# Performance work log

Hardware: AMD Instinct MI355X
Metric: run time of the kernel (lower is better)

## Reference

```python
import jax, jax.numpy as jnp
import numpy as np

N, E, C = 50000, 600000, 128
BN_EPS = 1e-5
NORM_EPS = 1e-12


def _edgeconv(x, src, dst, wa, ba, g, be, rm, rv, wb, bb):
    # PyG EdgeConv: message = MLP(concat(x_i, x_j - x_i)); aggr='add' at target i
    x_i = x[dst]                      # [E, C] target features
    x_j = x[src]                      # [E, C] source features
    m = jnp.concatenate([x_i, x_j - x_i], axis=-1)   # [E, 2C]
    m = jax.nn.relu(m @ wa.T + ba)                   # Linear(2C->C) + ReLU
    m = (m - rm) * (g * jax.lax.rsqrt(rv + BN_EPS)) + be  # BatchNorm1d (eval)
    m = m @ wb.T + bb                                # Linear(C->C)
    return jax.ops.segment_sum(m, dst, num_segments=x.shape[0])  # [N, C]


def _lin(k, fan_in, shape):
    bound = 1.0 / np.sqrt(fan_in)
    return jax.random.uniform(k, shape, jnp.float32, -bound, bound)


def setup_inputs() -> dict:
    key = jax.random.key(0)
    ks = jax.random.split(key, 16)
    inp = {
        "x": jax.random.normal(ks[0], (N, C), jnp.float32),
        "edge_index": jax.random.randint(ks[1], (2, E), 0, N, jnp.int64),
    }
    # layer 1 params
    inp["w1a"] = _lin(ks[2], 2 * C, (C, 2 * C)); inp["b1a"] = _lin(ks[3], 2 * C, (C,))
    inp["g1"] = jnp.ones((C,), jnp.float32) + 0.1 * jax.random.normal(ks[4], (C,))
    inp["be1"] = 0.1 * jax.random.normal(ks[5], (C,))
    inp["rm1"] = 0.1 * jax.random.normal(ks[6], (C,))
    inp["rv1"] = 0.5 + jax.random.uniform(ks[7], (C,))
    inp["w1b"] = _lin(ks[8], C, (C, C)); inp["b1b"] = _lin(ks[9], C, (C,))
    # layer 2 params
    inp["w2a"] = _lin(ks[10], 2 * C, (C, 2 * C)); inp["b2a"] = _lin(ks[11], 2 * C, (C,))
    inp["g2"] = jnp.ones((C,), jnp.float32) + 0.1 * jax.random.normal(ks[12], (C,))
    inp["be2"] = 0.1 * jax.random.normal(ks[13], (C,))
    inp["rm2"] = 0.1 * jax.random.normal(ks[14], (C,))
    inp["rv2"] = 0.5 + jax.random.uniform(ks[15], (C,))
    k2 = jax.random.split(ks[15], 2)
    inp["w2b"] = _lin(k2[0], C, (C, C)); inp["b2b"] = _lin(k2[1], C, (C,))
    return inp


def reference(x, edge_index, w1a, b1a, g1, be1, rm1, rv1, w1b, b1b,
              w2a, b2a, g2, be2, rm2, rv2, w2b, b2b):
    src, dst = edge_index[0], edge_index[1]
    # layer 1 (all but last): conv -> relu -> L2 normalize -> dropout(eval=identity)
    h = _edgeconv(x, src, dst, w1a, b1a, g1, be1, rm1, rv1, w1b, b1b)
    h = jax.nn.relu(h)
    h = h / jnp.maximum(jnp.linalg.norm(h, axis=-1, keepdims=True), NORM_EPS)
    # last layer: conv only
    return _edgeconv(h, src, dst, w2a, b2a, g2, be2, rm2, rv2, w2b, b2b)
```

## Files before the change

kernel.cpp:

```cpp
#include <hip/hip_runtime.h>

#define CCH 128
#define WPAD 136
typedef unsigned short ushort;
typedef __attribute__((ext_vector_type(8))) short bf16x8_t;
typedef __attribute__((ext_vector_type(4))) float f32x4;

union ABu { bf16x8_t v; ushort u[8]; uint4 q; };

__device__ __forceinline__ ushort f2b(float f) {
  union { float f; unsigned u; } v{f};
  unsigned r = v.u + 0x7fffu + ((v.u >> 16) & 1u);
  return (ushort)(r >> 16);
}
__device__ __forceinline__ float b2f(ushort s) {
  union { unsigned u; float f; } v{(unsigned)s << 16};
  return v.f;
}

__global__ __launch_bounds__(256) void k_pre(const float* __restrict__ x,
                                             ushort* __restrict__ XB, int nxc,
                                             const float* __restrict__ w1a,
                                             const float* __restrict__ w1b,
                                             const float* __restrict__ w2a,
                                             const float* __restrict__ w2b,
                                             ushort* __restrict__ Wcat1, ushort* __restrict__ Wb1,
                                             ushort* __restrict__ Wcat2, ushort* __restrict__ Wb2,
                                             const void* __restrict__ ei, int* __restrict__ deg,
                                             int E, int xcb) {
  const int b = blockIdx.x, t = threadIdx.x;
  if (b < 128) {
    int i = b * 256 + t;
    int c = i >> 7, k = i & 127;
    float v = (c < 128) ? w1a[c * 256 + k] - w1a[c * 256 + 128 + k]
                        : w1a[(c - 128) * 256 + 128 + k];
    Wcat1[i] = f2b(v);
    if (i < 16384) Wb1[i] = f2b(w1b[i]);
  } else if (b < 256) {
    int i = (b - 128) * 256 + t;
    int c = i >> 7, k = i & 127;
    float v = (c < 128) ? w2a[c * 256 + k] - w2a[c * 256 + 128 + k]
                        : w2a[(c - 128) * 256 + 128 + k];
    Wcat2[i] = f2b(v);
    if (i < 16384) Wb2[i] = f2b(w2b[i]);
  } else if (b < 256 + xcb) {
    size_t i = (size_t)(b - 256) * 256 + t;
    if (i < (size_t)nxc) {
      const float* xp = x + i * 8;
      float4 f0 = *(const float4*)xp;
      float4 f1 = *(const float4*)(xp + 4);
      ushort o[8] = {f2b(f0.x), f2b(f0.y), f2b(f0.z), f2b(f0.w),
                     f2b(f1.x), f2b(f1.y), f2b(f1.z), f2b(f1.w)};
      *(uint4*)&XB[i * 8] = *(const uint4*)o;
    }
  } else {
    __shared__ int nz;
    if (t == 0) nz = 0;
    __syncthreads();
    int e = (b - 256 - xcb) * 256 + t;
    unsigned hi = (e < E) ? ((const unsigned*)ei)[2 * (size_t)e + 1] : 0u;
    if (hi) atomicAdd(&nz, 1);
    __syncthreads();
    bool i64 = (nz == 0);
    if (e < E) {
      int d = i64 ? (int)((const long long*)ei)[(size_t)E + e]
                  : ((const int*)ei)[(size_t)E + e];
      atomicAdd(&deg[d], 1);
    }
  }
}

__global__ __launch_bounds__(256) void k_rowptr(const int* __restrict__ deg,
                                                const int* __restrict__ bsum,
                                                int* __restrict__ rowptr,
                                                int n, int nb, int Etot) {
  __shared__ int s[256];
  const int t = threadIdx.x, b = blockIdx.x;
  s[t] = (t < nb && t < b) ? bsum[t] : 0;
  __syncthreads();
  for (int off = 128; off > 0; off >>= 1) {
    if (t < off) s[t] += s[t + off];
    __syncthreads();
  }
  int boffset = s[0];
  __syncthreads();
  int i = b * 256 + t;
  int v = (i < n) ? deg[i] : 0;
  s[t] = v; __syncthreads();
  for (int off = 1; off < 256; off <<= 1) {
    int tv = (t >= off) ? s[t - off] : 0;
    __syncthreads();
    s[t] += tv;
    __syncthreads();
  }
  if (i < n) rowptr[i] = boffset + s[t] - v;
  if (b == gridDim.x - 1 && t == 0) rowptr[n] = Etot;
}

__global__ __launch_bounds__(256) void k_scatter(const void* __restrict__ ei,
                                                 const int* __restrict__ rowptr,
                                                 int* __restrict__ cnt,
                                                 int* __restrict__ esrc, int E) {
  __shared__ int nz;
  const int t = threadIdx.x;
  if (t == 0) nz = 0;
  __syncthreads();
  int e = blockIdx.x * 256 + t;
  unsigned hi = (e < E) ? ((const unsigned*)ei)[2 * (size_t)e + 1] : 0u;
  if (hi) atomicAdd(&nz, 1);
  __syncthreads();
  bool i64 = (nz == 0);
  if (e < E) {
    int d, sv;
    if (i64) {
      sv = (int)((const long long*)ei)[(size_t)e];
      d  = (int)((const long long*)ei)[(size_t)E + e];
    } else {
      sv = ((const int*)ei)[(size_t)e];
      d  = ((const int*)ei)[(size_t)E + e];
    }
    int pos = rowptr[d] + atomicAdd(&cnt[d], 1);
    esrc[pos] = sv;
  }
}

__device__ __forceinline__ void gemm_core(const ushort* __restrict__ XB,
                                          const ushort* __restrict__ wlds,
                                          int rowb, int ln, int quad, int nN,
                                          f32x4 acc0[8], f32x4 acc1[8]) {
  const int ar0 = rowb + ln, ar1 = rowb + 16 + ln;
  ABu a0[4], a1[4];
#pragma unroll
  for (int kk = 0; kk < 4; ++kk) {
    a0[kk].q = (ar0 < nN) ? *(const uint4*)(XB + (size_t)ar0 * CCH + kk * 32 + quad * 8)
                          : make_uint4(0, 0, 0, 0);
    a1[kk].q = (ar1 < nN) ? *(const uint4*)(XB + (size_t)ar1 * CCH + kk * 32 + quad * 8)
                          : make_uint4(0, 0, 0, 0);
  }
#pragma unroll
  for (int s = 0; s < 8; ++s) {
    acc0[s] = (f32x4){0.f, 0.f, 0.f, 0.f};
    acc1[s] = (f32x4){0.f, 0.f, 0.f, 0.f};
  }
#pragma unroll
  for (int s = 0; s < 8; ++s) {
#pragma unroll
    for (int kk = 0; kk < 4; ++kk) {
      ABu b;
      b.q = *(const uint4*)&wlds[(s * 16 + ln) * WPAD + kk * 32 + quad * 8];
      acc0[s] = __builtin_amdgcn_mfma_f32_16x16x32_bf16(a0[kk].v, b.v, acc0[s], 0, 0, 0);
      acc1[s] = __builtin_amdgcn_mfma_f32_16x16x32_bf16(a1[kk].v, b.v, acc1[s], 0, 0, 0);
    }
  }
}

__device__ __forceinline__ void stage_w(const ushort* __restrict__ Wp,
                                        ushort* __restrict__ wlds, int t) {
  for (int i = t; i < 128 * 16; i += 256) {
    int row = i >> 4, ch = i & 15;
    *(uint4*)&wlds[row * WPAD + ch * 8] = *(const uint4*)&Wp[row * CCH + ch * 8];
  }
}

__device__ __forceinline__ void epi0(f32x4 acc[8], int rowb, int ln, int quad, int nN,
                                     const float* bias, int half, ushort* dst) {
#pragma unroll
  for (int s = 0; s < 8; ++s) {
    int col = s * 16 + ln;
    float bv = half ? 0.f : bias[col];
#pragma unroll
    for (int r = 0; r < 4; ++r) {
      int row = rowb + quad * 4 + r;
      if (row < nN) dst[(size_t)row * CCH + col] = f2b(acc[s][r] + bv);
    }
  }
}

__global__ __launch_bounds__(256) void k_mix1(const ushort* __restrict__ XB,
                                              const ushort* __restrict__ Wcat,
                                              const float* __restrict__ bias,
                                              ushort* __restrict__ A1,
                                              ushort* __restrict__ A2, int nN,
                                              const int* __restrict__ deg,
                                              int* __restrict__ bsum, int gH, int n) {
  __shared__ ushort wlds[128 * WPAD];
  const int t = threadIdx.x;
  if ((int)blockIdx.x >= 2 * gH) {
    int* s = (int*)wlds;
    int bb = blockIdx.x - 2 * gH;
    int i = bb * 256 + t;
    s[t] = (i < n) ? deg[i] : 0;
    __syncthreads();
    for (int off = 128; off > 0; off >>= 1) {
      if (t < off) s[t] += s[t + off];
      __syncthreads();
    }
    if (t == 0) bsum[bb] = s[0];
    return;
  }
  const int half = (int)blockIdx.x >= gH;
  const int bx = half ? blockIdx.x - gH : blockIdx.x;
  stage_w(Wcat + (size_t)half * 128 * CCH, wlds, t);
  __syncthreads();
  const int wave = t >> 6, lane = t & 63;
  const int ln = lane & 15, quad = lane >> 4;
  const int rowb = bx * 128 + wave * 32;
  f32x4 acc0[8], acc1[8];
  gemm_core(XB, wlds, rowb, ln, quad, nN, acc0, acc1);
  ushort* dst = half ? A2 : A1;
  epi0(acc0, rowb, ln, quad, nN, bias, half, dst);
  epi0(acc1, rowb + 16, ln, quad, nN, bias, half, dst);
}

template <int EPI>
__global__ __launch_bounds__(256) void k_gemm(const ushort* __restrict__ XB,
                                              const ushort* __restrict__ W,
                                              const float* __restrict__ bias,
                                              const int* __restrict__ deg,
                                              void* __restrict__ Y1,
                                              ushort* __restrict__ Y2, int nN) {
  __shared__ ushort wlds[128 * WPAD];
  const int t = threadIdx.x;
  const int half = (EPI == 0) ? blockIdx.y : 0;
  stage_w(W + (size_t)half * 128 * CCH, wlds, t);
  __syncthreads();
  const int wave = t >> 6, lane = t & 63;
  const int ln = lane & 15, quad = lane >> 4;
  const int rowb = blockIdx.x * 128 + wave * 32;
  f32x4 acc0[8], acc1[8];
  gemm_core(XB, wlds, rowb, ln, quad, nN, acc0, acc1);

  if constexpr (EPI == 0) {
    ushort* dst = half ? Y2 : (ushort*)Y1;
    epi0(acc0, rowb, ln, quad, nN, bias, half, dst);
    epi0(acc1, rowb + 16, ln, quad, nN, bias, half, dst);
  } else if constexpr (EPI == 1) {
    ushort* H = (ushort*)Y1;
    float biasv[8];
#pragma unroll
    for (int s = 0; s < 8; ++s) biasv[s] = bias[s * 16 + ln];
    auto epi = [&](f32x4* acc, int rb) {
#pragma unroll
      for (int r = 0; r < 4; ++r) {
        int row = rb + quad * 4 + r;
        float dn = (row < nN) ? (float)deg[row] : 0.f;
        float vals[8];
        float ss = 0.f;
#pragma unroll
        for (int s = 0; s < 8; ++s) {
          float v = fmaxf(acc[s][r] + dn * biasv[s], 0.f);
          vals[s] = v;
          ss += v * v;
        }
        ss += __shfl_xor(ss, 1, 64);
        ss += __shfl_xor(ss, 2, 64);
        ss += __shfl_xor(ss, 4, 64);
        ss += __shfl_xor(ss, 8, 64);
        float inv = 1.0f / fmaxf(sqrtf(ss), 1e-12f);
        if (row < nN) {
#pragma unroll
          for (int s = 0; s < 8; ++s)
            H[(size_t)row * CCH + s * 16 + ln] = f2b(vals[s] * inv);
        }
      }
    };
    epi(acc0, rowb); epi(acc1, rowb + 16);
  } else {
    float* OUT = (float*)Y1;
    float biasv[8];
#pragma unroll
    for (int s = 0; s < 8; ++s) biasv[s] = bias[s * 16 + ln];
    auto epi = [&](f32x4* acc, int rb) {
#pragma unroll
      for (int r = 0; r < 4; ++r) {
        int row = rb + quad * 4 + r;
        if (row >= nN) continue;
        float dn = (float)deg[row];
#pragma unroll
        for (int s = 0; s < 8; ++s)
          OUT[(size_t)row * CCH + s * 16 + ln] = acc[s][r] + dn * biasv[s];
      }
    };
    epi(acc0, rowb); epi(acc1, rowb + 16);
  }
}

__global__ __launch_bounds__(256) void k_aggr(const ushort* __restrict__ A1,
                                              const ushort* __restrict__ A2,
                                              const int* __restrict__ rowptr,
                                              const int* __restrict__ esrc,
                                              const float* __restrict__ g,
                                              const float* __restrict__ be,
                                              const float* __restrict__ rm,
                                              const float* __restrict__ rv,
                                              ushort* __restrict__ M, int nNodes) {
  int node = blockIdx.x * 4 + (threadIdx.x >> 6);
  if (node >= nNodes) return;
  int lane = threadIdx.x & 63;
  int q = lane >> 4;
  int c = (lane & 15) * 8;

  uint4 aq = *(const uint4*)&A1[(size_t)node * CCH + c];
  float a[8] = {b2f((ushort)aq.x), b2f((ushort)(aq.x >> 16)),
                b2f((ushort)aq.y), b2f((ushort)(aq.y >> 16)),
                b2f((ushort)aq.z), b2f((ushort)(aq.z >> 16)),
                b2f((ushort)aq.w), b2f((ushort)(aq.w >> 16))};
  int r0 = rowptr[node], r1 = rowptr[node + 1];
  float s[8] = {0.f, 0.f, 0.f, 0.f, 0.f, 0.f, 0.f, 0.f};

  auto acc8 = [&](uint4 w) {
    const unsigned* p = (const unsigned*)&w;
#pragma unroll
    for (int j = 0; j < 4; ++j) {
      s[2*j]   += fmaxf(a[2*j]   + b2f((ushort)p[j]), 0.f);
      s[2*j+1] += fmaxf(a[2*j+1] + b2f((ushort)(p[j] >> 16)), 0.f);
    }
  };

  for (int base = r0; base < r1; base += 64) {
    int navail = r1 - base; if (navail > 64) navail = 64;
    int myi = (lane < navail) ? esrc[base + lane] : 0;
    int g4 = navail >> 2, tail = navail & 3;
    int j = 0;
    for (; j + 4 <= g4; j += 4) {
      int p0 = j * 4 + q;
      int i0 = __shfl(myi, p0, 64);
      int i1 = __shfl(myi, p0 + 4, 64);
      int i2 = __shfl(myi, p0 + 8, 64);
      int i3 = __shfl(myi, p0 + 12, 64);
      uint4 w0 = *(const uint4*)&A2[(size_t)i0 * CCH + c];
      uint4 w1 = *(const uint4*)&A2[(size_t)i1 * CCH + c];
      uint4 w2 = *(const uint4*)&A2[(size_t)i2 * CCH + c];
      uint4 w3 = *(const uint4*)&A2[(size_t)i3 * CCH + c];
      acc8(w0); acc8(w1); acc8(w2); acc8(w3);
    }
    for (; j < g4; ++j) {
      int i0 = __shfl(myi, j * 4 + q, 64);
      acc8(*(const uint4*)&A2[(size_t)i0 * CCH + c]);
    }
    int pt = g4 * 4 + q; if (pt > 63) pt = 63;
    int it = __shfl(myi, pt, 64);
    if (q < tail) acc8(*(const uint4*)&A2[(size_t)it * CCH + c]);
  }
#pragma unroll
  for (int j = 0; j < 8; ++j) {
    s[j] += __shfl_xor(s[j], 16, 64);
    s[j] += __shfl_xor(s[j], 32, 64);
  }

  if (q == 0) {
    float dn = (float)(r1 - r0);
    unsigned p[4];
#pragma unroll
    for (int j = 0; j < 4; ++j) {
      float sc0 = g[c + 2*j]     * rsqrtf(rv[c + 2*j]     + 1e-5f);
      float sc1 = g[c + 2*j + 1] * rsqrtf(rv[c + 2*j + 1] + 1e-5f);
      float o0 = sc0 * s[2*j]     + dn * (be[c + 2*j]     - rm[c + 2*j]     * sc0);
      float o1 = sc1 * s[2*j + 1] + dn * (be[c + 2*j + 1] - rm[c + 2*j + 1] * sc1);
      p[j] = (unsigned)f2b(o0) | ((unsigned)f2b(o1) << 16);
    }
    *(uint4*)&M[(size_t)node * CCH + c] = make_uint4(p[0], p[1], p[2], p[3]);
  }
}

extern "C" void kernel_launch(void* const* d_in, const int* in_sizes, int n_in,
                              void* d_out, int out_size, void* d_ws, size_t ws_size,
                              hipStream_t stream) {
  const float* x   = (const float*)d_in[0];
  const void*  ei  = d_in[1];
  const float* w1a = (const float*)d_in[2];
  const float* b1a = (const float*)d_in[3];
  const float* g1  = (const float*)d_in[4];
  const float* be1 = (const float*)d_in[5];
  const float* rm1 = (const float*)d_in[6];
  const float* rv1 = (const float*)d_in[7];
  const float* w1b = (const float*)d_in[8];
  const float* b1b = (const float*)d_in[9];
  const float* w2a = (const float*)d_in[10];
  const float* b2a = (const float*)d_in[11];
  const float* g2  = (const float*)d_in[12];
  const float* be2 = (const float*)d_in[13];
  const float* rm2 = (const float*)d_in[14];
  const float* rv2 = (const float*)d_in[15];
  const float* w2b = (const float*)d_in[16];
  const float* b2b = (const float*)d_in[17];

  const int N = in_sizes[0] / CCH;
  const int E = in_sizes[1] / 2;
  const size_t NC = (size_t)N * CCH;

  int* deg    = (int*)d_ws;
  int* cnt    = deg + N;
  int* rowptr = cnt + N;
  int* bsum   = rowptr + N + 1;
  int* esrc   = bsum + 256;
  uintptr_t pw = ((uintptr_t)(esrc + E) + 63) & ~(uintptr_t)63;
  ushort* Wcat1 = (ushort*)pw;
  ushort* Wcat2 = Wcat1 + 32768;
  ushort* Wb1   = Wcat2 + 32768;
  ushort* Wb2   = Wb1 + 16384;
  uintptr_t pb = ((uintptr_t)(Wb2 + 16384) + 63) & ~(uintptr_t)63;
  ushort* XB = (ushort*)pb;
  ushort* B0 = XB + NC;
  ushort* B1 = B0 + NC;
  ushort* MB = B1 + NC;
  ushort* HB = MB + NC;

  const int gE  = (E + 255) / 256;
  const int gS  = (N + 255) / 256;
  const int gH  = (N + 127) / 128;
  const int gA  = (N + 3) / 4;
  const int nxc = (int)(NC / 8);
  const int xcb = (nxc + 255) / 256;

  hipMemsetAsync(deg, 0, sizeof(int) * 2 * (size_t)N, stream);
  k_pre<<<256 + xcb + gE, 256, 0, stream>>>(x, XB, nxc, w1a, w1b, w2a, w2b,
                                            Wcat1, Wb1, Wcat2, Wb2, ei, deg, E, xcb);
  k_mix1<<<2 * gH + gS, 256, 0, stream>>>(XB, Wcat1, b1a, B0, B1, N, deg, bsum, gH, N);
  k_rowptr<<<gS, 256, 0, stream>>>(deg, bsum, rowptr, N, gS, E);
  k_scatter<<<gE, 256, 0, stream>>>(ei, rowptr, cnt, esrc, E);

  k_aggr<<<gA, 256, 0, stream>>>(B0, B1, rowptr, esrc, g1, be1, rm1, rv1, MB, N);
  k_gemm<1><<<gH, 256, 0, stream>>>(MB, Wb1, b1b, deg, HB, nullptr, N);
  k_gemm<0><<<dim3(gH, 2), 256, 0, stream>>>(HB, Wcat2, b2a, deg, B0, B1, N);
  k_aggr<<<gA, 256, 0, stream>>>(B0, B1, rowptr, esrc, g2, be2, rm2, rv2, MB, N);
  k_gemm<2><<<gH, 256, 0, stream>>>(MB, Wb2, b2b, deg, d_out, nullptr, N);
}
```

Measured before the change: 299.3 us.

## Fuse fp32 input conversion into first GEMM and fuse layer-1 output GEMM with layer-2 input GEMM

Drops the separate x-to-bf16 conversion pass: k_mix1 now reads fp32 x and converts it in registers, and one block computes both weight halves so the A fragments are loaded once. Layer 1's Linear(C->C) with ReLU and L2-normalise now shares a kernel with layer 2's first GEMM. The normalised H stays in LDS rather than making a round trip through global memory, which also removes one launch. In exchange each block does more serial work, reuses the weight LDS buffer across stages with extra barriers, and k_fuse12 needs twice the LDS, which may lower occupancy.

Result: no change. 296.6 us (-0.9%).

```diff
diff --git a/kernel.cpp b/kernel.cpp
--- a/kernel.cpp
+++ b/kernel.cpp
@@ -18,16 +18,14 @@
   return v.f;
 }
 
-__global__ __launch_bounds__(256) void k_pre(const float* __restrict__ x,
-                                             ushort* __restrict__ XB, int nxc,
-                                             const float* __restrict__ w1a,
+__global__ __launch_bounds__(256) void k_pre(const float* __restrict__ w1a,
                                              const float* __restrict__ w1b,
                                              const float* __restrict__ w2a,
                                              const float* __restrict__ w2b,
                                              ushort* __restrict__ Wcat1, ushort* __restrict__ Wb1,
                                              ushort* __restrict__ Wcat2, ushort* __restrict__ Wb2,
                                              const void* __restrict__ ei, int* __restrict__ deg,
-                                             int E, int xcb) {
+                                             int E) {
   const int b = blockIdx.x, t = threadIdx.x;
   if (b < 128) {
     int i = b * 256 + t;
@@ -43,21 +41,11 @@
                         : w2a[(c - 128) * 256 + 128 + k];
     Wcat2[i] = f2b(v);
     if (i < 16384) Wb2[i] = f2b(w2b[i]);
-  } else if (b < 256 + xcb) {
-    size_t i = (size_t)(b - 256) * 256 + t;
-    if (i < (size_t)nxc) {
-      const float* xp = x + i * 8;
-      float4 f0 = *(const float4*)xp;
-      float4 f1 = *(const float4*)(xp + 4);
-      ushort o[8] = {f2b(f0.x), f2b(f0.y), f2b(f0.z), f2b(f0.w),
-                     f2b(f1.x), f2b(f1.y), f2b(f1.z), f2b(f1.w)};
-      *(uint4*)&XB[i * 8] = *(const uint4*)o;
-    }
   } else {
     __shared__ int nz;
     if (t == 0) nz = 0;
     __syncthreads();
-    int e = (b - 256 - xcb) * 256 + t;
+    int e = (b - 256) * 256 + t;
     unsigned hi = (e < E) ? ((const unsigned*)ei)[2 * (size_t)e + 1] : 0u;
     if (hi) atomicAdd(&nz, 1);
     __syncthreads();
@@ -124,12 +112,17 @@
   }
 }
 
-__device__ __forceinline__ void gemm_core(const ushort* __restrict__ XB,
-                                          const ushort* __restrict__ wlds,
-                                          int rowb, int ln, int quad, int nN,
-                                          f32x4 acc0[8], f32x4 acc1[8]) {
-  const int ar0 = rowb + ln, ar1 = rowb + 16 + ln;
-  ABu a0[4], a1[4];
+__device__ __forceinline__ void stage_w(const ushort* __restrict__ Wp,
+                                        ushort* __restrict__ wlds, int t) {
+  for (int i = t; i < 128 * 16; i += 256) {
+    int row = i >> 4, ch = i & 15;
+    *(uint4*)&wlds[row * WPAD + ch * 8] = *(const uint4*)&Wp[row * CCH + ch * 8];
+  }
+}
+
+__device__ __forceinline__ void load_a_bf16(const ushort* __restrict__ XB,
+                                            int ar0, int ar1, int quad, int nN,
+                                            ABu a0[4], ABu a1[4]) {
 #pragma unroll
   for (int kk = 0; kk < 4; ++kk) {
     a0[kk].q = (ar0 < nN) ? *(const uint4*)(XB + (size_t)ar0 * CCH + kk * 32 + quad * 8)
@@ -137,6 +130,46 @@
     a1[kk].q = (ar1 < nN) ? *(const uint4*)(XB + (size_t)ar1 * CCH + kk * 32 + quad * 8)
                           : make_uint4(0, 0, 0, 0);
   }
+}
+
+__device__ __forceinline__ void load_a_f32(const float* __restrict__ X,
+                                           int ar0, int ar1, int quad, int nN,
+                                           ABu a0[4], ABu a1[4]) {
+#pragma unroll
+  for (int kk = 0; kk < 4; ++kk) {
+    if (ar0 < nN) {
+      const float* p = X + (size_t)ar0 * CCH + kk * 32 + quad * 8;
+      float4 f0 = *(const float4*)p, f1 = *(const float4*)(p + 4);
+      a0[kk].u[0] = f2b(f0.x); a0[kk].u[1] = f2b(f0.y);
+      a0[kk].u[2] = f2b(f0.z); a0[kk].u[3] = f2b(f0.w);
+      a0[kk].u[4] = f2b(f1.x); a0[kk].u[5] = f2b(f1.y);
+      a0[kk].u[6] = f2b(f1.z); a0[kk].u[7] = f2b(f1.w);
+    } else a0[kk].q = make_uint4(0, 0, 0, 0);
+    if (ar1 < nN) {
+      const float* p = X + (size_t)ar1 * CCH + kk * 32 + quad * 8;
+      float4 f0 = *(const float4*)p, f1 = *(const float4*)(p + 4);
+      a1[kk].u[0] = f2b(f0.x); a1[kk].u[1] = f2b(f0.y);
+      a1[kk].u[2] = f2b(f0.z); a1[kk].u[3] = f2b(f0.w);
+      a1[kk].u[4] = f2b(f1.x); a1[kk].u[5] = f2b(f1.y);
+      a1[kk].u[6] = f2b(f1.z); a1[kk].u[7] = f2b(f1.w);
+    } else a1[kk].q = make_uint4(0, 0, 0, 0);
+  }
+}
+
+__device__ __forceinline__ void load_a_lds(const ushort* __restrict__ hlds,
+                                           int lr0, int lr1, int quad,
+                                           ABu a0[4], ABu a1[4]) {
+#pragma unroll
+  for (int kk = 0; kk < 4; ++kk) {
+    a0[kk].q = *(const uint4*)&hlds[lr0 * WPAD + kk * 32 + quad * 8];
+    a1[kk].q = *(const uint4*)&hlds[lr1 * WPAD + kk * 32 + quad * 8];
+  }
+}
+
+__device__ __forceinline__ void mma_tiles(const ABu a0[4], const ABu a1[4],
+                                          const ushort* __restrict__ wlds,
+                                          int ln, int quad,
+                                          f32x4 acc0[8], f32x4 acc1[8]) {
 #pragma unroll
   for (int s = 0; s < 8; ++s) {
     acc0[s] = (f32x4){0.f, 0.f, 0.f, 0.f};
@@ -154,14 +187,6 @@
   }
 }
 
-__device__ __forceinline__ void stage_w(const ushort* __restrict__ Wp,
-                                        ushort* __restrict__ wlds, int t) {
-  for (int i = t; i < 128 * 16; i += 256) {
-    int row = i >> 4, ch = i & 15;
-    *(uint4*)&wlds[row * WPAD + ch * 8] = *(const uint4*)&Wp[row * CCH + ch * 8];
-  }
-}
-
 __device__ __forceinline__ void epi0(f32x4 acc[8], int rowb, int ln, int quad, int nN,
                                      const float* bias, int half, ushort* dst) {
 #pragma unroll
@@ -176,7 +201,7 @@
   }
 }
 
-__global__ __launch_bounds__(256) void k_mix1(const ushort* __restrict__ XB,
+__global__ __launch_bounds__(256) void k_mix1(const float* __restrict__ x,
                                               const ushort* __restrict__ Wcat,
                                               const float* __restrict__ bias,
                                               ushort* __restrict__ A1,
@@ -185,9 +210,9 @@
                                               int* __restrict__ bsum, int gH, int n) {
   __shared__ ushort wlds[128 * WPAD];
   const int t = threadIdx.x;
-  if ((int)blockIdx.x >= 2 * gH) {
+  if ((int)blockIdx.x >= gH) {
     int* s = (int*)wlds;
-    int bb = blockIdx.x - 2 * gH;
+    int bb = blockIdx.x - gH;
     int i = bb * 256 + t;
     s[t] = (i < n) ? deg[i] : 0;
     __syncthreads();
@@ -198,91 +223,125 @@
     if (t == 0) bsum[bb] = s[0];
     return;
   }
-  const int half = (int)blockIdx.x >= gH;
-  const int bx = half ? blockIdx.x - gH : blockIdx.x;
-  stage_w(Wcat + (size_t)half * 128 * CCH, wlds, t);
-  __syncthreads();
-  const int wave = t >> 6, lane = t & 63;
-  const int ln = lane & 15, quad = lane >> 4;
-  const int rowb = bx * 128 + wave * 32;
-  f32x4 acc0[8], acc1[8];
-  gemm_core(XB, wlds, rowb, ln, quad, nN, acc0, acc1);
-  ushort* dst = half ? A2 : A1;
-  epi0(acc0, rowb, ln, quad, nN, bias, half, dst);
-  epi0(acc1, rowb + 16, ln, quad, nN, bias, half, dst);
-}
-
-template <int EPI>
-__global__ __launch_bounds__(256) void k_gemm(const ushort* __restrict__ XB,
-                                              const ushort* __restrict__ W,
-                                              const float* __restrict__ bias,
-                                              const int* __restrict__ deg,
-                                              void* __restrict__ Y1,
-                                              ushort* __restrict__ Y2, int nN) {
-  __shared__ ushort wlds[128 * WPAD];
-  const int t = threadIdx.x;
-  const int half = (EPI == 0) ? blockIdx.y : 0;
-  stage_w(W + (size_t)half * 128 * CCH, wlds, t);
-  __syncthreads();
   const int wave = t >> 6, lane = t & 63;
   const int ln = lane & 15, quad = lane >> 4;
   const int rowb = blockIdx.x * 128 + wave * 32;
+  stage_w(Wcat, wlds, t);
+  ABu a0[4], a1[4];
+  load_a_f32(x, rowb + ln, rowb + 16 + ln, quad, nN, a0, a1);
+  __syncthreads();
   f32x4 acc0[8], acc1[8];
-  gemm_core(XB, wlds, rowb, ln, quad, nN, acc0, acc1);
-
-  if constexpr (EPI == 0) {
-    ushort* dst = half ? Y2 : (ushort*)Y1;
-    epi0(acc0, rowb, ln, quad, nN, bias, half, dst);
-    epi0(acc1, rowb + 16, ln, quad, nN, bias, half, dst);
-  } else if constexpr (EPI == 1) {
-    ushort* H = (ushort*)Y1;
-    float biasv[8];
-#pragma unroll
-    for (int s = 0; s < 8; ++s) biasv[s] = bias[s * 16 + ln];
-    auto epi = [&](f32x4* acc, int rb) {
-#pragma unroll
-      for (int r = 0; r < 4; ++r) {
-        int row = rb + quad * 4 + r;
-        float dn = (row < nN) ? (float)deg[row] : 0.f;
-        float vals[8];
-        float ss = 0.f;
-#pragma unroll
-        for (int s = 0; s < 8; ++s) {
-          float v = fmaxf(acc[s][r] + dn * biasv[s], 0.f);
-          vals[s] = v;
-          ss += v * v;
-        }
-        ss += __shfl_xor(ss, 1, 64);
-        ss += __shfl_xor(ss, 2, 64);
-        ss += __shfl_xor(ss, 4, 64);
-        ss += __shfl_xor(ss, 8, 64);
-        float inv = 1.0f / fmaxf(sqrtf(ss), 1e-12f);
-        if (row < nN) {
-#pragma unroll
-          for (int s = 0; s < 8; ++s)
-            H[(size_t)row * CCH + s * 16 + ln] = f2b(vals[s] * inv);
-        }
+  mma_tiles(a0, a1, wlds, ln, quad, acc0, acc1);
+  epi0(acc0, rowb, ln, quad, nN, bias, 0, A1);
+  epi0(acc1, rowb + 16, ln, quad, nN, bias, 0, A1);
+  __syncthreads();
+  stage_w(Wcat + 128 * CCH, wlds, t);
+  __syncthreads();
+  mma_tiles(a0, a1, wlds, ln, quad, acc0, acc1);
+  epi0(acc0, rowb, ln, quad, nN, bias, 1, A2);
+  epi0(acc1, rowb + 16, ln, quad, nN, bias, 1, A2);
+}
+
+__global__ __launch_bounds__(256) void k_fuse12(const ushort* __restrict__ MB,
+                                                const ushort* __restrict__ Wb1,
+                                                const float* __restrict__ b1b,
+                                                const ushort* __restrict__ Wcat2,
+                                                const float* __restrict__ b2a,
+                                                const int* __restrict__ deg,
+                                                ushort* __restrict__ B0,
+                                                ushort* __restrict__ B1, int nN) {
+  __shared__ ushort wlds[128 * WPAD];
+  __shared__ ushort hlds[128 * WPAD];
+  const int t = threadIdx.x, wave = t >> 6, lane = t & 63;
+  const int ln = lane & 15, quad = lane >> 4;
+  const int rowb = blockIdx.x * 128 + wave * 32;
+  const int lrb = wave * 32;
+
+  stage_w(Wb1, wlds, t);
+  ABu a0[4], a1[4];
+  load_a_bf16(MB, rowb + ln, rowb + 16 + ln, quad, nN, a0, a1);
+  __syncthreads();
+  f32x4 acc0[8], acc1[8];
+  mma_tiles(a0, a1, wlds, ln, quad, acc0, acc1);
+
+  float biasv[8];
+#pragma unroll
+  for (int s = 0; s < 8; ++s) biasv[s] = b1b[s * 16 + ln];
+  auto epiH = [&](f32x4* acc, int rb, int lb) {
+#pragma unroll
+    for (int r = 0; r < 4; ++r) {
+      int row = rb + quad * 4 + r;
+      int lrow = lb + quad * 4 + r;
+      float dn = (row < nN) ? (float)deg[row] : 0.f;
+      float vals[8];
+      float ss = 0.f;
+#pragma unroll
+      for (int s = 0; s < 8; ++s) {
+        float v = fmaxf(acc[s][r] + dn * biasv[s], 0.f);
+        vals[s] = v;
+        ss += v * v;
       }
-    };
-    epi(acc0, rowb); epi(acc1, rowb + 16);
-  } else {
-    float* OUT = (float*)Y1;
-    float biasv[8];
-#pragma unroll
-    for (int s = 0; s < 8; ++s) biasv[s] = bias[s * 16 + ln];
-    auto epi = [&](f32x4* acc, int rb) {
-#pragma unroll
-      for (int r = 0; r < 4; ++r) {
-        int row = rb + quad * 4 + r;
-        if (row >= nN) continue;
-        float dn = (float)deg[row];
-#pragma unroll
-        for (int s = 0; s < 8; ++s)
-          OUT[(size_t)row * CCH + s * 16 + ln] = acc[s][r] + dn * biasv[s];
-      }
-    };
-    epi(acc0, rowb); epi(acc1, rowb + 16);
-  }
+      ss += __shfl_xor(ss, 1, 64);
+      ss += __shfl_xor(ss, 2, 64);
+      ss += __shfl_xor(ss, 4, 64);
+      ss += __shfl_xor(ss, 8, 64);
+      float inv = 1.0f / fmaxf(sqrtf(ss), 1e-12f);
+#pragma unroll
+      for (int s = 0; s < 8; ++s)
+        hlds[lrow * WPAD + s * 16 + ln] = (row < nN) ? f2b(vals[s] * inv) : (ushort)0;
+    }
+  };
+  epiH(acc0, rowb, lrb);
+  epiH(acc1, rowb + 16, lrb + 16);
+  __syncthreads();
+
+  stage_w(Wcat2, wlds, t);
+  load_a_lds(hlds, lrb + ln, lrb + 16 + ln, quad, a0, a1);
+  __syncthreads();
+  mma_tiles(a0, a1, wlds, ln, quad, acc0, acc1);
+  epi0(acc0, rowb, ln, quad, nN, b2a, 0, B0);
+  epi0(acc1, rowb + 16, ln, quad, nN, b2a, 0, B0);
+  __syncthreads();
+
+  stage_w(Wcat2 + 128 * CCH, wlds, t);
+  __syncthreads();
+  mma_tiles(a0, a1, wlds, ln, quad, acc0, acc1);
+  epi0(acc0, rowb, ln, quad, nN, b2a, 1, B1);
+  epi0(acc1, rowb + 16, ln, quad, nN, b2a, 1, B1);
+}
+
+__global__ __launch_bounds__(256) void k_gemmf(const ushort* __restrict__ XB,
+                                               const ushort* __restrict__ W,
+                                               const float* __restrict__ bias,
+                                               const int* __restrict__ deg,
+                                               float* __restrict__ OUT, int nN) {
+  __shared__ ushort wlds[128 * WPAD];
+  const int t = threadIdx.x;
+  stage_w(W, wlds, t);
+  const int wave = t >> 6, lane = t & 63;
+  const int ln = lane & 15, quad = lane >> 4;
+  const int rowb = blockIdx.x * 128 + wave * 32;
+  ABu a0[4], a1[4];
+  load_a_bf16(XB, rowb + ln, rowb + 16 + ln, quad, nN, a0, a1);
+  __syncthreads();
+  f32x4 acc0[8], acc1[8];
+  mma_tiles(a0, a1, wlds, ln, quad, acc0, acc1);
+  float biasv[8];
+#pragma unroll
+  for (int s = 0; s < 8; ++s) biasv[s] = bias[s * 16 + ln];
+  auto epi = [&](f32x4* acc, int rb) {
+#pragma unroll
+    for (int r = 0; r < 4; ++r) {
+      int row = rb + quad * 4 + r;
+      if (row >= nN) continue;
+      float dn = (float)deg[row];
+#pragma unroll
+      for (int s = 0; s < 8; ++s)
+        OUT[(size_t)row * CCH + s * 16 + ln] = acc[s][r] + dn * biasv[s];
+    }
+  };
+  epi(acc0, rowb);
+  epi(acc1, rowb + 16);
 }
 
 __global__ __launch_bounds__(256) void k_aggr(const ushort* __restrict__ A1,
@@ -400,29 +459,24 @@
   ushort* Wb1   = Wcat2 + 32768;
   ushort* Wb2   = Wb1 + 16384;
   uintptr_t pb = ((uintptr_t)(Wb2 + 16384) + 63) & ~(uintptr_t)63;
-  ushort* XB = (ushort*)pb;
-  ushort* B0 = XB + NC;
+  ushort* B0 = (ushort*)pb;
   ushort* B1 = B0 + NC;
   ushort* MB = B1 + NC;
-  ushort* HB = MB + NC;
 
   const int gE  = (E + 255) / 256;
   const int gS  = (N + 255) / 256;
   const int gH  = (N + 127) / 128;
   const int gA  = (N + 3) / 4;
-  const int nxc = (int)(NC / 8);
-  const int xcb = (nxc + 255) / 256;
 
   hipMemsetAsync(deg, 0, sizeof(int) * 2 * (size_t)N, stream);
-  k_pre<<<256 + xcb + gE, 256, 0, stream>>>(x, XB, nxc, w1a, w1b, w2a, w2b,
-                                            Wcat1, Wb1, Wcat2, Wb2, ei, deg, E, xcb);
-  k_mix1<<<2 * gH + gS, 256, 0, stream>>>(XB, Wcat1, b1a, B0, B1, N, deg, bsum, gH, N);
+  k_pre<<<256 + gE, 256, 0, stream>>>(w1a, w1b, w2a, w2b,
+                                      Wcat1, Wb1, Wcat2, Wb2, ei, deg, E);
+  k_mix1<<<gH + gS, 256, 0, stream>>>(x, Wcat1, b1a, B0, B1, N, deg, bsum, gH, N);
   k_rowptr<<<gS, 256, 0, stream>>>(deg, bsum, rowptr, N, gS, E);
   k_scatter<<<gE, 256, 0, stream>>>(ei, rowptr, cnt, esrc, E);
 
   k_aggr<<<gA, 256, 0, stream>>>(B0, B1, rowptr, esrc, g1, be1, rm1, rv1, MB, N);
-  k_gemm<1><<<gH, 256, 0, stream>>>(MB, Wb1, b1b, deg, HB, nullptr, N);
-  k_gemm<0><<<dim3(gH, 2), 256, 0, stream>>>(HB, Wcat2, b2a, deg, B0, B1, N);
+  k_fuse12<<<gH, 256, 0, stream>>>(MB, Wb1, b1b, Wcat2, b2a, deg, B0, B1, N);
   k_aggr<<<gA, 256, 0, stream>>>(B0, B1, rowptr, esrc, g2, be2, rm2, rv2, MB, N);
-  k_gemm<2><<<gH, 256, 0, stream>>>(MB, Wb2, b2b, deg, d_out, nullptr, N);
-}
+  k_gemmf<<<gH, 256, 0, stream>>>(MB, Wb2, b2b, deg, (float*)d_out, N);
+}
```
